# Performance work log

Hardware: AMD Instinct MI355X
Metric: run time of the kernel (lower is better)

## Reference

```python
import jax, jax.numpy as jnp
import numpy as np

B, H, S, D = 2, 16, 2048, 64  # depth = dmodel / num_heads
DMODEL = H * D


def setup_inputs() -> dict:
    key = jax.random.key(0)
    kq, kk, kv, kw = jax.random.split(key, 4)
    Q = jax.random.normal(kq, (B, H, S, D), dtype=jnp.float32)
    K = jax.random.normal(kk, (B, H, S, D), dtype=jnp.float32)
    V = jax.random.normal(kv, (B, H, S, D), dtype=jnp.float32)
    W = jax.random.normal(kw, (DMODEL, DMODEL), dtype=jnp.float32) * (1.0 / np.sqrt(DMODEL))
    b = jnp.zeros((DMODEL,), dtype=jnp.float32)
    return {"Q": Q, "K": K, "V": V, "W": W, "b": b}


def reference(Q, K, V, W, b):
    depth = Q.shape[-1]
    # scores: (B, H, S, S) -- full score matrix, matching the original math
    scores = jnp.einsum('bhqd,bhkd->bhqk', Q, K) / jnp.sqrt(jnp.float32(depth))
    attn = jax.nn.softmax(scores, axis=-1)
    vals = jnp.einsum('bhqk,bhkd->bhqd', attn, V)          # (B, H, S, D)
    vals = jnp.transpose(vals, (0, 2, 1, 3))               # (B, S, H, D)
    concat = vals.reshape(vals.shape[0], vals.shape[1], -1)  # (B, S, dmodel)
    return concat @ W + b
```

## Files before the change

### kernel.cpp

```cpp
#include <hip/hip_runtime.h>
#include <hip/hip_bf16.h>


typedef float  f32x16 __attribute__((ext_vector_type(16)));
typedef float  f32x4v __attribute__((ext_vector_type(4)));
typedef float  f32x2v __attribute__((ext_vector_type(2)));
typedef __bf16 bf16x8 __attribute__((ext_vector_type(8)));
typedef __bf16 bf16x4 __attribute__((ext_vector_type(4)));
typedef __bf16 bf16x2 __attribute__((ext_vector_type(2)));

static constexpr int Bn = 2, Hn = 16, Sn = 2048, Dn = 64, DM = 1024;
static constexpr size_t QKV_ELEMS = (size_t)Bn * Hn * Sn * Dn;

#define QSCALE 0.18033688011112042f

#if __has_builtin(__builtin_amdgcn_cvt_pk_bf16_f32)
static __device__ __forceinline__ unsigned pack2(float a, float b) {
  bf16x2 t = __builtin_amdgcn_cvt_pk_bf16_f32(a, b);
  union { bf16x2 v; unsigned u; } c; c.v = t; return c.u;
}
#else
static __device__ __forceinline__ unsigned pack2(float a, float b) {
  union { __bf16 h; unsigned short s; } ua, ub;
  ua.h = (__bf16)a; ub.h = (__bf16)b;
  return (unsigned)ua.s | ((unsigned)ub.s << 16);
}
#endif

static __device__ __forceinline__ void unzip8(const unsigned* wds, bf16x8* r0, bf16x8* r1) {
  union { unsigned u[4]; bf16x8 v; } a, b;
#pragma unroll
  for (int i = 0; i < 4; ++i) {
    unsigned lo = wds[2 * i], hi = wds[2 * i + 1];
    a.u[i] = (lo & 0xffffu) | (hi << 16);
    b.u[i] = (lo >> 16) | (hi & 0xffff0000u);
  }
  *r0 = a.v; *r1 = b.v;
}

__global__ __launch_bounds__(256) void convert_qk(
    const float* __restrict__ q, const float* __restrict__ k,
    __bf16* __restrict__ qo, __bf16* __restrict__ ko) {
  const int z = blockIdx.y;
  const float* src = z ? k : q;
  __bf16* dst      = z ? ko : qo;
  const float scale = z ? 1.0f : QSCALE;
  size_t i = ((size_t)blockIdx.x * 256 + threadIdx.x) * 8;
  f32x4v a = *(const f32x4v*)(src + i);
  f32x4v b = *(const f32x4v*)(src + i + 4);
  bf16x8 o;
#pragma unroll
  for (int j = 0; j < 4; ++j) { o[j] = (__bf16)(a[j] * scale); o[4 + j] = (__bf16)(b[j] * scale); }
  *(bf16x8*)(dst + i) = o;
}

__global__ __launch_bounds__(256) void convert_vt(const float* __restrict__ v,
                                                  __bf16* __restrict__ vt) {
  __shared__ __bf16 T[64][74];
  const int t = threadIdx.x, r = t >> 2, c0 = (t & 3) * 16;
  const int kv0 = blockIdx.x * 64, bh = blockIdx.y;
  const float* src = v + ((size_t)bh * Sn + kv0 + r) * Dn + c0;
  union { bf16x8 v8; unsigned u[4]; } o0, o1;
#pragma unroll
  for (int i = 0; i < 2; ++i) {
    f32x4v f = *(const f32x4v*)(src + i * 4);
#pragma unroll
    for (int j = 0; j < 4; ++j) o0.v8[i * 4 + j] = (__bf16)f[j];
  }
#pragma unroll
  for (int i = 0; i < 2; ++i) {
    f32x4v f = *(const f32x4v*)(src + 8 + i * 4);
#pragma unroll
    for (int j = 0; j < 4; ++j) o1.v8[i * 4 + j] = (__bf16)f[j];
  }
#pragma unroll
  for (int j = 0; j < 4; ++j) {
    *(unsigned*)&T[r][c0 + 2 * j]     = o0.u[j];
    *(unsigned*)&T[r][c0 + 8 + 2 * j] = o1.u[j];
  }
  __syncthreads();
  const int rp = t >> 3, k0 = (t & 7) * 8;
  unsigned wds[8];
#pragma unroll
  for (int i = 0; i < 8; ++i) wds[i] = *(const unsigned*)&T[k0 + i][2 * rp];
  bf16x8 r0, r1; unzip8(wds, &r0, &r1);
  __bf16* dst = vt + ((size_t)bh * Dn + 2 * rp) * Sn + kv0 + k0;
  *(bf16x8*)dst = r0;
  *(bf16x8*)(dst + Sn) = r1;
}

__global__ __launch_bounds__(256) void convert_w(const float* __restrict__ w,
                                                 __bf16* __restrict__ wt) {
  __shared__ __bf16 T[64][74];
  const int t = threadIdx.x, r = t >> 2, c0 = (t & 3) * 16;
  const int nt = blockIdx.x * 64, kt = blockIdx.y * 64;
  const float* src = w + (size_t)(kt + r) * DM + nt + c0;
  union { bf16x8 v8; unsigned u[4]; } o0, o1;
#pragma unroll
  for (int i = 0; i < 2; ++i) {
    f32x4v f = *(const f32x4v*)(src + i * 4);
#pragma unroll
    for (int j = 0; j < 4; ++j) o0.v8[i * 4 + j] = (__bf16)f[j];
  }
#pragma unroll
  for (int i = 0; i < 2; ++i) {
    f32x4v f = *(const f32x4v*)(src + 8 + i * 4);
#pragma unroll
    for (int j = 0; j < 4; ++j) o1.v8[i * 4 + j] = (__bf16)f[j];
  }
#pragma unroll
  for (int j = 0; j < 4; ++j) {
    *(unsigned*)&T[r][c0 + 2 * j]     = o0.u[j];
    *(unsigned*)&T[r][c0 + 8 + 2 * j] = o1.u[j];
  }
  __syncthreads();
  const int rp = t >> 3, k0 = (t & 7) * 8;
  unsigned wds[8];
#pragma unroll
  for (int i = 0; i < 8; ++i) wds[i] = *(const unsigned*)&T[k0 + i][2 * rp];
  bf16x8 r0, r1; unzip8(wds, &r0, &r1);
  __bf16* dst = wt + (size_t)(nt + 2 * rp) * DM + kt + k0;
  *(bf16x8*)dst = r0;
  *(bf16x8*)(dst + DM) = r1;
}

__global__ __launch_bounds__(256, 4) void attn(
    const __bf16* __restrict__ Qb, const __bf16* __restrict__ Kb,
    const __bf16* __restrict__ Vtg, __bf16* __restrict__ Cc) {
  const int tid = threadIdx.x;
  const int wave = tid >> 6, lane = tid & 63;
  const int ln = lane & 31, g = lane >> 5;
  const int qb = blockIdx.x, h = blockIdx.y, bz = blockIdx.z;

  __shared__ __bf16 Ks[2][64][72];
  __shared__ __bf16 Vs[2][64][72];

  const size_t hoff = (size_t)(bz * Hn + h) * Sn * Dn;
  const __bf16* Qp = Qb + hoff + (size_t)(qb * 128 + wave * 32) * Dn;
  const __bf16* Kp = Kb + hoff;
  const __bf16* Vp = Vtg + hoff;

  bf16x8 qf[4];
#pragma unroll
  for (int ks = 0; ks < 4; ++ks)
    qf[ks] = *(const bf16x8*)(Qp + (size_t)ln * Dn + ks * 16 + g * 8);

  const int sr = tid >> 2, sc = (tid & 3) * 16;
  const __bf16* kbase = Kp + (size_t)sr * Dn + sc;
  const __bf16* vbase = Vp + (size_t)sr * Sn + sc;

  bf16x8 k0r = *(const bf16x8*)kbase, k1r = *(const bf16x8*)(kbase + 8);
  bf16x8 v0r = *(const bf16x8*)vbase, v1r = *(const bf16x8*)(vbase + 8);
  *(bf16x8*)&Ks[0][sr][sc]     = k0r;
  *(bf16x8*)&Ks[0][sr][sc + 8] = k1r;
  *(bf16x8*)&Vs[0][sr][sc]     = v0r;
  *(bf16x8*)&Vs[0][sr][sc + 8] = v1r;
  k0r = *(const bf16x8*)(kbase + (size_t)64 * Dn);
  k1r = *(const bf16x8*)(kbase + (size_t)64 * Dn + 8);
  v0r = *(const bf16x8*)(vbase + 64);
  v1r = *(const bf16x8*)(vbase + 64 + 8);
  __syncthreads();

  f32x16 O0 = {}, O1 = {};
  float Lown = 0.0f;
  constexpr int NT = Sn / 64;

  for (int kt = 0; kt < NT; ++kt) {
    const int buf = kt & 1;

    float p[32];
#pragma unroll
    for (int mt = 0; mt < 2; ++mt) {
      f32x16 s = {};
#pragma unroll
      for (int ks = 0; ks < 4; ++ks) {
        bf16x8 kf = *(const bf16x8*)&Ks[buf][mt * 32 + ln][ks * 16 + g * 8];
        s = __builtin_amdgcn_mfma_f32_32x32x16_bf16(kf, qf[ks], s, 0, 0, 0);
      }
#pragma unroll
      for (int r = 0; r < 16; ++r) p[mt * 16 + r] = __builtin_amdgcn_exp2f(s[r]);
    }
    f32x2v s2 = {0.0f, 0.0f};
#pragma unroll
    for (int tt = 0; tt < 16; ++tt) {
      f32x2v t2 = {p[2 * tt], p[2 * tt + 1]};
      s2 += t2;
    }
    Lown += s2[0] + s2[1];

    unsigned w[16];
#pragma unroll
    for (int tt = 0; tt < 8; ++tt) {
      w[tt]     = pack2(p[2 * tt], p[2 * tt + 1]);
      w[8 + tt] = pack2(p[16 + 2 * tt], p[16 + 2 * tt + 1]);
    }

    if (kt + 1 < NT) {
      const int nb = buf ^ 1;
      *(bf16x8*)&Ks[nb][sr][sc]     = k0r;
      *(bf16x8*)&Ks[nb][sr][sc + 8] = k1r;
      *(bf16x8*)&Vs[nb][sr][sc]     = v0r;
      *(bf16x8*)&Vs[nb][sr][sc + 8] = v1r;
      if (kt + 2 < NT) {
        const __bf16* kp = kbase + (size_t)(kt + 2) * 64 * Dn;
        k0r = *(const bf16x8*)kp; k1r = *(const bf16x8*)(kp + 8);
        const __bf16* vp = vbase + (kt + 2) * 64;
        v0r = *(const bf16x8*)vp; v1r = *(const bf16x8*)(vp + 8);
      }
    }

#pragma unroll
    for (int s4 = 0; s4 < 4; ++s4) {
      const int wb = (s4 >> 1) * 8 + (s4 & 1) * 4;
      unsigned xs0 = g ? w[wb + 0] : w[wb + 2];
      unsigned xs1 = g ? w[wb + 1] : w[wb + 3];
      unsigned x0 = (unsigned)__shfl_xor((int)xs0, 32);
      unsigned x1 = (unsigned)__shfl_xor((int)xs1, 32);
      union { unsigned u[4]; bf16x8 v; } pu;
      pu.u[0] = g ? x0 : w[wb + 0];
      pu.u[1] = g ? x1 : w[wb + 1];
      pu.u[2] = g ? w[wb + 2] : x0;
      pu.u[3] = g ? w[wb + 3] : x1;
      bf16x8 vf0 = *(const bf16x8*)&Vs[buf][ln][s4 * 16 + g * 8];
      bf16x8 vf1 = *(const bf16x8*)&Vs[buf][32 + ln][s4 * 16 + g * 8];
      O0 = __builtin_amdgcn_mfma_f32_32x32x16_bf16(vf0, pu.v, O0, 0, 0, 0);
      O1 = __builtin_amdgcn_mfma_f32_32x32x16_bf16(vf1, pu.v, O1, 0, 0, 0);
    }
    __syncthreads();
  }

  const float Lfull = Lown + __shfl_xor(Lown, 32);
  const float inv = 1.0f / Lfull;
  __bf16* Osb = ((__bf16*)Ks) + wave * 32 * 72;
#pragma unroll
  for (int mtD = 0; mtD < 2; ++mtD) {
#pragma unroll
    for (int a = 0; a < 4; ++a) {
      const f32x16 O = mtD ? O1 : O0;
      bf16x4 t4;
#pragma unroll
      for (int c = 0; c < 4; ++c) t4[c] = (__bf16)(O[4 * a + c] * inv);
      *(bf16x4*)(Osb + ln * 72 + mtD * 32 + 8 * a + 4 * g) = t4;
    }
  }
  const int q0w = qb * 128 + wave * 32;
#pragma unroll
  for (int i = 0; i < 4; ++i) {
    const int rq = i * 8 + (lane >> 3);
    const int c8 = (lane & 7) * 8;
    bf16x8 o = *(const bf16x8*)(Osb + rq * 72 + c8);
    size_t base = (((size_t)bz * Sn + q0w + rq) * Hn + h) * Dn + c8;
    *(bf16x8*)&Cc[base] = o;
  }
}

__global__ __launch_bounds__(256, 2) void proj(
    const __bf16* __restrict__ A, const __bf16* __restrict__ Wt,
    const float* __restrict__ bias, float* __restrict__ out) {
  const int tid = threadIdx.x, wave = tid >> 6, lane = tid & 63;
  const int ln = lane & 31, g = lane >> 5;
  const int bm = blockIdx.x, bn = blockIdx.y;
  __shared__ __bf16 As[2][128][72];
  __shared__ __bf16 Bs[2][64][72];
  const int ar = tid >> 1, ac = (tid & 1) * 32;
  const int br = tid >> 2, bc = (tid & 3) * 16;
  f32x16 acc0 = {}, acc1 = {};
  const __bf16* Ap = A + (size_t)(bm * 128) * DM;
  const __bf16* Wp = Wt + (size_t)(bn * 64) * DM;

  bf16x8 a0, a1, a2, a3, b0, b1;
  {
    const __bf16* ap = Ap + (size_t)ar * DM + ac;
    a0 = *(const bf16x8*)ap;        a1 = *(const bf16x8*)(ap + 8);
    a2 = *(const bf16x8*)(ap + 16); a3 = *(const bf16x8*)(ap + 24);
    const __bf16* wp = Wp + (size_t)br * DM + bc;
    b0 = *(const bf16x8*)wp; b1 = *(const bf16x8*)(wp + 8);
  }
  *(bf16x8*)&As[0][ar][ac]      = a0;
  *(bf16x8*)&As[0][ar][ac + 8]  = a1;
  *(bf16x8*)&As[0][ar][ac + 16] = a2;
  *(bf16x8*)&As[0][ar][ac + 24] = a3;
  *(bf16x8*)&Bs[0][br][bc]      = b0;
  *(bf16x8*)&Bs[0][br][bc + 8]  = b1;
  {
    const __bf16* ap = Ap + (size_t)ar * DM + 64 + ac;
    a0 = *(const bf16x8*)ap;        a1 = *(const bf16x8*)(ap + 8);
    a2 = *(const bf16x8*)(ap + 16); a3 = *(const bf16x8*)(ap + 24);
    const __bf16* wp = Wp + (size_t)br * DM + 64 + bc;
    b0 = *(const bf16x8*)wp; b1 = *(const bf16x8*)(wp + 8);
  }
  __syncthreads();

  constexpr int KT = DM / 64;
  for (int kt = 0; kt < KT; ++kt) {
    const int buf = kt & 1;
#pragma unroll
    for (int ks = 0; ks < 4; ++ks) {
      bf16x8 af  = *(const bf16x8*)&As[buf][wave * 32 + ln][ks * 16 + g * 8];
      bf16x8 wf0 = *(const bf16x8*)&Bs[buf][ln][ks * 16 + g * 8];
      bf16x8 wf1 = *(const bf16x8*)&Bs[buf][32 + ln][ks * 16 + g * 8];
      acc0 = __builtin_amdgcn_mfma_f32_32x32x16_bf16(af, wf0, acc0, 0, 0, 0);
      acc1 = __builtin_amdgcn_mfma_f32_32x32x16_bf16(af, wf1, acc1, 0, 0, 0);
    }
    if (kt + 1 < KT) {
      const int nb = buf ^ 1;
      *(bf16x8*)&As[nb][ar][ac]      = a0;
      *(bf16x8*)&As[nb][ar][ac + 8]  = a1;
      *(bf16x8*)&As[nb][ar][ac + 16] = a2;
      *(bf16x8*)&As[nb][ar][ac + 24] = a3;
      *(bf16x8*)&Bs[nb][br][bc]      = b0;
      *(bf16x8*)&Bs[nb][br][bc + 8]  = b1;
      if (kt + 2 < KT) {
        const __bf16* ap = Ap + (size_t)ar * DM + (kt + 2) * 64 + ac;
        a0 = *(const bf16x8*)ap;        a1 = *(const bf16x8*)(ap + 8);
        a2 = *(const bf16x8*)(ap + 16); a3 = *(const bf16x8*)(ap + 24);
        const __bf16* wp = Wp + (size_t)br * DM + (kt + 2) * 64 + bc;
        b0 = *(const bf16x8*)wp; b1 = *(const bf16x8*)(wp + 8);
      }
    }
    __syncthreads();
  }
  float bv0 = bias[bn * 64 + ln], bv1 = bias[bn * 64 + 32 + ln];
#pragma unroll
  for (int r = 0; r < 16; ++r) {
    int row = bm * 128 + wave * 32 + (r & 3) + ((r >> 2) << 3) + (g << 2);
    out[(size_t)row * DM + bn * 64 + ln]      = acc0[r] + bv0;
    out[(size_t)row * DM + bn * 64 + 32 + ln] = acc1[r] + bv1;
  }
}

extern "C" void kernel_launch(void* const* d_in, const int* in_sizes, int n_in,
                              void* d_out, int out_size, void* d_ws, size_t ws_size,
                              hipStream_t stream) {
  const float* Q = (const float*)d_in[0];
  const float* K = (const float*)d_in[1];
  const float* V = (const float*)d_in[2];
  const float* W = (const float*)d_in[3];
  const float* b = (const float*)d_in[4];
  float* out = (float*)d_out;

  __bf16* ws  = (__bf16*)d_ws;
  __bf16* Qb  = ws;
  __bf16* Kb  = Qb + QKV_ELEMS;
  __bf16* Vtg = Kb + QKV_ELEMS;
  __bf16* Cc  = Vtg + QKV_ELEMS;
  __bf16* Wt  = Cc + QKV_ELEMS;

  convert_qk<<<dim3((unsigned)(QKV_ELEMS / (256 * 8)), 2, 1), 256, 0, stream>>>(Q, K, Qb, Kb);
  convert_vt<<<dim3(Sn / 64, Bn * Hn, 1), 256, 0, stream>>>(V, Vtg);
  convert_w<<<dim3(DM / 64, DM / 64, 1), 256, 0, stream>>>(W, Wt);
  attn<<<dim3(Sn / 128, Hn, Bn), 256, 0, stream>>>(Qb, Kb, Vtg, Cc);
  proj<<<dim3(Bn * Sn / 128, DM / 64, 1), 256, 0, stream>>>(Cc, Wt, b, out);
}
```

Baseline: 163.6 us.

## Split attention KV tiles across wave pairs and shrink projection tiles

```diff
diff --git a/kernel.cpp b/kernel.cpp
--- a/kernel.cpp
+++ b/kernel.cpp
@@ -124,19 +124,21 @@
   *(bf16x8*)(dst + DM) = r1;
 }
 
-__global__ __launch_bounds__(256, 4) void attn(
+__global__ __launch_bounds__(512, 4) void attn(
     const __bf16* __restrict__ Qb, const __bf16* __restrict__ Kb,
     const __bf16* __restrict__ Vtg, __bf16* __restrict__ Cc) {
   const int tid = threadIdx.x;
   const int wave = tid >> 6, lane = tid & 63;
   const int ln = lane & 31, g = lane >> 5;
+  const int qg = wave >> 1, kh = wave & 1;
   const int qb = blockIdx.x, h = blockIdx.y, bz = blockIdx.z;
 
-  __shared__ __bf16 Ks[2][64][72];
-  __shared__ __bf16 Vs[2][64][72];
+  __shared__ __bf16 smem[2][2][64][72];
+  __bf16 (*Ks)[64][72] = smem[0];
+  __bf16 (*Vs)[64][72] = smem[1];
 
   const size_t hoff = (size_t)(bz * Hn + h) * Sn * Dn;
-  const __bf16* Qp = Qb + hoff + (size_t)(qb * 128 + wave * 32) * Dn;
+  const __bf16* Qp = Qb + hoff + (size_t)(qb * 128 + qg * 32) * Dn;
   const __bf16* Kp = Kb + hoff;
   const __bf16* Vp = Vtg + hoff;
 
@@ -145,20 +147,16 @@
   for (int ks = 0; ks < 4; ++ks)
     qf[ks] = *(const bf16x8*)(Qp + (size_t)ln * Dn + ks * 16 + g * 8);
 
-  const int sr = tid >> 2, sc = (tid & 3) * 16;
+  const int sr = tid >> 3, sc = (tid & 7) * 8;
   const __bf16* kbase = Kp + (size_t)sr * Dn + sc;
   const __bf16* vbase = Vp + (size_t)sr * Sn + sc;
 
-  bf16x8 k0r = *(const bf16x8*)kbase, k1r = *(const bf16x8*)(kbase + 8);
-  bf16x8 v0r = *(const bf16x8*)vbase, v1r = *(const bf16x8*)(vbase + 8);
-  *(bf16x8*)&Ks[0][sr][sc]     = k0r;
-  *(bf16x8*)&Ks[0][sr][sc + 8] = k1r;
-  *(bf16x8*)&Vs[0][sr][sc]     = v0r;
-  *(bf16x8*)&Vs[0][sr][sc + 8] = v1r;
+  bf16x8 k0r = *(const bf16x8*)kbase;
+  bf16x8 v0r = *(const bf16x8*)vbase;
+  *(bf16x8*)&Ks[0][sr][sc] = k0r;
+  *(bf16x8*)&Vs[0][sr][sc] = v0r;
   k0r = *(const bf16x8*)(kbase + (size_t)64 * Dn);
-  k1r = *(const bf16x8*)(kbase + (size_t)64 * Dn + 8);
   v0r = *(const bf16x8*)(vbase + 64);
-  v1r = *(const bf16x8*)(vbase + 64 + 8);
   __syncthreads();
 
   f32x16 O0 = {}, O1 = {};
@@ -168,50 +166,37 @@
   for (int kt = 0; kt < NT; ++kt) {
     const int buf = kt & 1;
 
-    float p[32];
-#pragma unroll
-    for (int mt = 0; mt < 2; ++mt) {
-      f32x16 s = {};
-#pragma unroll
-      for (int ks = 0; ks < 4; ++ks) {
-        bf16x8 kf = *(const bf16x8*)&Ks[buf][mt * 32 + ln][ks * 16 + g * 8];
-        s = __builtin_amdgcn_mfma_f32_32x32x16_bf16(kf, qf[ks], s, 0, 0, 0);
-      }
-#pragma unroll
-      for (int r = 0; r < 16; ++r) p[mt * 16 + r] = __builtin_amdgcn_exp2f(s[r]);
-    }
+    f32x16 s = {};
+#pragma unroll
+    for (int ks = 0; ks < 4; ++ks) {
+      bf16x8 kf = *(const bf16x8*)&Ks[buf][kh * 32 + ln][ks * 16 + g * 8];
+      s = __builtin_amdgcn_mfma_f32_32x32x16_bf16(kf, qf[ks], s, 0, 0, 0);
+    }
+    float p[16];
+#pragma unroll
+    for (int r = 0; r < 16; ++r) p[r] = __builtin_amdgcn_exp2f(s[r]);
     f32x2v s2 = {0.0f, 0.0f};
 #pragma unroll
-    for (int tt = 0; tt < 16; ++tt) {
-      f32x2v t2 = {p[2 * tt], p[2 * tt + 1]};
-      s2 += t2;
-    }
+    for (int tt = 0; tt < 8; ++tt) { f32x2v t2 = {p[2 * tt], p[2 * tt + 1]}; s2 += t2; }
     Lown += s2[0] + s2[1];
 
-    unsigned w[16];
-#pragma unroll
-    for (int tt = 0; tt < 8; ++tt) {
-      w[tt]     = pack2(p[2 * tt], p[2 * tt + 1]);
-      w[8 + tt] = pack2(p[16 + 2 * tt], p[16 + 2 * tt + 1]);
-    }
+    unsigned w[8];
+#pragma unroll
+    for (int tt = 0; tt < 8; ++tt) w[tt] = pack2(p[2 * tt], p[2 * tt + 1]);
 
     if (kt + 1 < NT) {
       const int nb = buf ^ 1;
-      *(bf16x8*)&Ks[nb][sr][sc]     = k0r;
-      *(bf16x8*)&Ks[nb][sr][sc + 8] = k1r;
-      *(bf16x8*)&Vs[nb][sr][sc]     = v0r;
-      *(bf16x8*)&Vs[nb][sr][sc + 8] = v1r;
+      *(bf16x8*)&Ks[nb][sr][sc] = k0r;
+      *(bf16x8*)&Vs[nb][sr][sc] = v0r;
       if (kt + 2 < NT) {
-        const __bf16* kp = kbase + (size_t)(kt + 2) * 64 * Dn;
-        k0r = *(const bf16x8*)kp; k1r = *(const bf16x8*)(kp + 8);
-        const __bf16* vp = vbase + (kt + 2) * 64;
-        v0r = *(const bf16x8*)vp; v1r = *(const bf16x8*)(vp + 8);
+        k0r = *(const bf16x8*)(kbase + (size_t)(kt + 2) * 64 * Dn);
+        v0r = *(const bf16x8*)(vbase + (kt + 2) * 64);
       }
     }
 
 #pragma unroll
-    for (int s4 = 0; s4 < 4; ++s4) {
-      const int wb = (s4 >> 1) * 8 + (s4 & 1) * 4;
+    for (int s4 = 0; s4 < 2; ++s4) {
+      const int wb = s4 * 4;
       unsigned xs0 = g ? w[wb + 0] : w[wb + 2];
       unsigned xs1 = g ? w[wb + 1] : w[wb + 3];
       unsigned x0 = (unsigned)__shfl_xor((int)xs0, 32);
@@ -221,72 +206,103 @@
       pu.u[1] = g ? x1 : w[wb + 1];
       pu.u[2] = g ? w[wb + 2] : x0;
       pu.u[3] = g ? w[wb + 3] : x1;
-      bf16x8 vf0 = *(const bf16x8*)&Vs[buf][ln][s4 * 16 + g * 8];
-      bf16x8 vf1 = *(const bf16x8*)&Vs[buf][32 + ln][s4 * 16 + g * 8];
+      bf16x8 vf0 = *(const bf16x8*)&Vs[buf][ln][kh * 32 + s4 * 16 + g * 8];
+      bf16x8 vf1 = *(const bf16x8*)&Vs[buf][32 + ln][kh * 32 + s4 * 16 + g * 8];
       O0 = __builtin_amdgcn_mfma_f32_32x32x16_bf16(vf0, pu.v, O0, 0, 0, 0);
       O1 = __builtin_amdgcn_mfma_f32_32x32x16_bf16(vf1, pu.v, O1, 0, 0, 0);
     }
     __syncthreads();
   }
 
-  const float Lfull = Lown + __shfl_xor(Lown, 32);
-  const float inv = 1.0f / Lfull;
-  __bf16* Osb = ((__bf16*)Ks) + wave * 32 * 72;
-#pragma unroll
-  for (int mtD = 0; mtD < 2; ++mtD) {
-#pragma unroll
-    for (int a = 0; a < 4; ++a) {
-      const f32x16 O = mtD ? O1 : O0;
-      bf16x4 t4;
-#pragma unroll
-      for (int c = 0; c < 4; ++c) t4[c] = (__bf16)(O[4 * a + c] * inv);
-      *(bf16x4*)(Osb + ln * 72 + mtD * 32 + 8 * a + 4 * g) = t4;
-    }
-  }
-  const int q0w = qb * 128 + wave * 32;
-#pragma unroll
-  for (int i = 0; i < 4; ++i) {
-    const int rq = i * 8 + (lane >> 3);
+  const float Lred = Lown + __shfl_xor(Lown, 32);
+  float* Ex = (float*)smem;
+  const int slot = (qg * 64 + lane) * 36;
+  if (kh == 1) {
+#pragma unroll
+    for (int i = 0; i < 4; ++i) {
+      f32x4v t = {O0[4 * i], O0[4 * i + 1], O0[4 * i + 2], O0[4 * i + 3]};
+      *(f32x4v*)&Ex[slot + 4 * i] = t;
+    }
+#pragma unroll
+    for (int i = 0; i < 4; ++i) {
+      f32x4v t = {O1[4 * i], O1[4 * i + 1], O1[4 * i + 2], O1[4 * i + 3]};
+      *(f32x4v*)&Ex[slot + 16 + 4 * i] = t;
+    }
+    Ex[slot + 32] = Lred;
+  }
+  __syncthreads();
+  float inv = 0.0f;
+  if (kh == 0) {
+#pragma unroll
+    for (int i = 0; i < 4; ++i) {
+      f32x4v t = *(const f32x4v*)&Ex[slot + 4 * i];
+#pragma unroll
+      for (int c = 0; c < 4; ++c) O0[4 * i + c] += t[c];
+    }
+#pragma unroll
+    for (int i = 0; i < 4; ++i) {
+      f32x4v t = *(const f32x4v*)&Ex[slot + 16 + 4 * i];
+#pragma unroll
+      for (int c = 0; c < 4; ++c) O1[4 * i + c] += t[c];
+    }
+    inv = 1.0f / (Lred + Ex[slot + 32]);
+  }
+  __syncthreads();
+  __bf16* T = (__bf16*)smem;
+  if (kh == 0) {
+#pragma unroll
+    for (int dh = 0; dh < 2; ++dh) {
+#pragma unroll
+      for (int a = 0; a < 4; ++a) {
+        const f32x16 O = dh ? O1 : O0;
+        bf16x4 t4;
+#pragma unroll
+        for (int c = 0; c < 4; ++c) t4[c] = (__bf16)(O[4 * a + c] * inv);
+        *(bf16x4*)&T[(qg * 32 + ln) * 72 + dh * 32 + 8 * a + 4 * g] = t4;
+      }
+    }
+  }
+  __syncthreads();
+  const int q0 = qb * 128;
+#pragma unroll
+  for (int i = 0; i < 2; ++i) {
+    const int rq = wave * 16 + i * 8 + (lane >> 3);
     const int c8 = (lane & 7) * 8;
-    bf16x8 o = *(const bf16x8*)(Osb + rq * 72 + c8);
-    size_t base = (((size_t)bz * Sn + q0w + rq) * Hn + h) * Dn + c8;
+    bf16x8 o = *(const bf16x8*)&T[rq * 72 + c8];
+    size_t base = (((size_t)bz * Sn + q0 + rq) * Hn + h) * Dn + c8;
     *(bf16x8*)&Cc[base] = o;
   }
 }
 
-__global__ __launch_bounds__(256, 2) void proj(
+__global__ __launch_bounds__(256, 4) void proj(
     const __bf16* __restrict__ A, const __bf16* __restrict__ Wt,
     const float* __restrict__ bias, float* __restrict__ out) {
   const int tid = threadIdx.x, wave = tid >> 6, lane = tid & 63;
   const int ln = lane & 31, g = lane >> 5;
+  const int mh = wave >> 1, nh = wave & 1;
   const int bm = blockIdx.x, bn = blockIdx.y;
-  __shared__ __bf16 As[2][128][72];
+  __shared__ __bf16 As[2][64][72];
   __shared__ __bf16 Bs[2][64][72];
-  const int ar = tid >> 1, ac = (tid & 1) * 32;
-  const int br = tid >> 2, bc = (tid & 3) * 16;
-  f32x16 acc0 = {}, acc1 = {};
-  const __bf16* Ap = A + (size_t)(bm * 128) * DM;
+  const int ar = tid >> 2, ac = (tid & 3) * 16;
+  f32x16 acc = {};
+  const __bf16* Ap = A + (size_t)(bm * 64) * DM;
   const __bf16* Wp = Wt + (size_t)(bn * 64) * DM;
 
-  bf16x8 a0, a1, a2, a3, b0, b1;
+  bf16x8 a0, a1, b0, b1;
   {
     const __bf16* ap = Ap + (size_t)ar * DM + ac;
-    a0 = *(const bf16x8*)ap;        a1 = *(const bf16x8*)(ap + 8);
-    a2 = *(const bf16x8*)(ap + 16); a3 = *(const bf16x8*)(ap + 24);
-    const __bf16* wp = Wp + (size_t)br * DM + bc;
+    a0 = *(const bf16x8*)ap; a1 = *(const bf16x8*)(ap + 8);
+    const __bf16* wp = Wp + (size_t)ar * DM + ac;
     b0 = *(const bf16x8*)wp; b1 = *(const bf16x8*)(wp + 8);
   }
-  *(bf16x8*)&As[0][ar][ac]      = a0;
-  *(bf16x8*)&As[0][ar][ac + 8]  = a1;
-  *(bf16x8*)&As[0][ar][ac + 16] = a2;
-  *(bf16x8*)&As[0][ar][ac + 24] = a3;
-  *(bf16x8*)&Bs[0][br][bc]      = b0;
-  *(bf16x8*)&Bs[0][br][bc + 8]  = b1;
+  *(bf16x8*)&As[0][ar][ac]     = a0;
+  *(bf16x8*)&As[0][ar][ac + 8] = a1;
+  *(bf16x8*)&Bs[0][ar][ac]     = b0;
+  *(bf16x8*)&Bs[0][ar][ac + 8] = b1;
   {
     const __bf16* ap = Ap + (size_t)ar * DM + 64 + ac;
-    a0 = *(const bf16x8*)ap;        a1 = *(const bf16x8*)(ap + 8);
-    a2 = *(const bf16x8*)(ap + 16); a3 = *(const bf16x8*)(ap + 24);
-    const __bf16* wp = Wp + (size_t)br * DM + 64 + bc;
+    a0 = *(const bf16x8*)ap; a1 = *(const bf16x8*)(ap + 8);
+    const __bf16* wp = Wp + (size_t)ar * DM + 64 + ac;
     b0 = *(const bf16x8*)wp; b1 = *(const bf16x8*)(wp + 8);
   }
   __syncthreads();
@@ -296,36 +312,30 @@
     const int buf = kt & 1;
 #pragma unroll
     for (int ks = 0; ks < 4; ++ks) {
-      bf16x8 af  = *(const bf16x8*)&As[buf][wave * 32 + ln][ks * 16 + g * 8];
-      bf16x8 wf0 = *(const bf16x8*)&Bs[buf][ln][ks * 16 + g * 8];
-      bf16x8 wf1 = *(const bf16x8*)&Bs[buf][32 + ln][ks * 16 + g * 8];
-      acc0 = __builtin_amdgcn_mfma_f32_32x32x16_bf16(af, wf0, acc0, 0, 0, 0);
-      acc1 = __builtin_amdgcn_mfma_f32_32x32x16_bf16(af, wf1, acc1, 0, 0, 0);
+      bf16x8 af = *(const bf16x8*)&As[buf][mh * 32 + ln][ks * 16 + g * 8];
+      bf16x8 wf = *(const bf16x8*)&Bs[buf][nh * 32 + ln][ks * 16 + g * 8];
+      acc = __builtin_amdgcn_mfma_f32_32x32x16_bf16(af, wf, acc, 0, 0, 0);
     }
     if (kt + 1 < KT) {
       const int nb = buf ^ 1;
-      *(bf16x8*)&As[nb][ar][ac]      = a0;
-      *(bf16x8*)&As[nb][ar][ac + 8]  = a1;
-      *(bf16x8*)&As[nb][ar][ac + 16] = a2;
-      *(bf16x8*)&As[nb][ar][ac + 24] = a3;
-      *(bf16x8*)&Bs[nb][br][bc]      = b0;
-      *(bf16x8*)&Bs[nb][br][bc + 8]  = b1;
+      *(bf16x8*)&As[nb][ar][ac]     = a0;
+      *(bf16x8*)&As[nb][ar][ac + 8] = a1;
+      *(bf16x8*)&Bs[nb][ar][ac]     = b0;
+      *(bf16x8*)&Bs[nb][ar][ac + 8] = b1;
       if (kt + 2 < KT) {
         const __bf16* ap = Ap + (size_t)ar * DM + (kt + 2) * 64 + ac;
-        a0 = *(const bf16x8*)ap;        a1 = *(const bf16x8*)(ap + 8);
-        a2 = *(const bf16x8*)(ap + 16); a3 = *(const bf16x8*)(ap + 24);
-        const __bf16* wp = Wp + (size_t)br * DM + (kt + 2) * 64 + bc;
+        a0 = *(const bf16x8*)ap; a1 = *(const bf16x8*)(ap + 8);
+        const __bf16* wp = Wp + (size_t)ar * DM + (kt + 2) * 64 + ac;
         b0 = *(const bf16x8*)wp; b1 = *(const bf16x8*)(wp + 8);
       }
     }
     __syncthreads();
   }
-  float bv0 = bias[bn * 64 + ln], bv1 = bias[bn * 64 + 32 + ln];
+  const float bv = bias[bn * 64 + nh * 32 + ln];
 #pragma unroll
   for (int r = 0; r < 16; ++r) {
-    int row = bm * 128 + wave * 32 + (r & 3) + ((r >> 2) << 3) + (g << 2);
-    out[(size_t)row * DM + bn * 64 + ln]      = acc0[r] + bv0;
-    out[(size_t)row * DM + bn * 64 + 32 + ln] = acc1[r] + bv1;
+    int row = bm * 64 + mh * 32 + (r & 3) + 8 * (r >> 2) + 4 * g;
+    out[(size_t)row * DM + bn * 64 + nh * 32 + ln] = acc[r] + bv;
   }
 }
 
@@ -349,6 +359,6 @@
   convert_qk<<<dim3((unsigned)(QKV_ELEMS / (256 * 8)), 2, 1), 256, 0, stream>>>(Q, K, Qb, Kb);
   convert_vt<<<dim3(Sn / 64, Bn * Hn, 1), 256, 0, stream>>>(V, Vtg);
   convert_w<<<dim3(DM / 64, DM / 64, 1), 256, 0, stream>>>(W, Wt);
-  attn<<<dim3(Sn / 128, Hn, Bn), 256, 0, stream>>>(Qb, Kb, Vtg, Cc);
-  proj<<<dim3(Bn * Sn / 128, DM / 64, 1), 256, 0, stream>>>(Cc, Wt, b, out);
-}
+  attn<<<dim3(Sn / 128, Hn, Bn), 512, 0, stream>>>(Qb, Kb, Vtg, Cc);
+  proj<<<dim3(Bn * Sn / 64, DM / 64, 1), 256, 0, stream>>>(Cc, Wt, b, out);
+}
```

Result: no change. 164.8 us (+0.8%).

## Split attention waves across query groups and key halves; fuse conversion kernels

Applied to the files above, without the earlier changes.

```diff
diff --git a/kernel.cpp b/kernel.cpp
--- a/kernel.cpp
+++ b/kernel.cpp
@@ -38,45 +38,66 @@
   *r0 = a.v; *r1 = b.v;
 }
 
-__global__ __launch_bounds__(256) void convert_qk(
+__global__ __launch_bounds__(256) void convert_all(
     const float* __restrict__ q, const float* __restrict__ k,
-    __bf16* __restrict__ qo, __bf16* __restrict__ ko) {
-  const int z = blockIdx.y;
-  const float* src = z ? k : q;
-  __bf16* dst      = z ? ko : qo;
-  const float scale = z ? 1.0f : QSCALE;
-  size_t i = ((size_t)blockIdx.x * 256 + threadIdx.x) * 8;
-  f32x4v a = *(const f32x4v*)(src + i);
-  f32x4v b = *(const f32x4v*)(src + i + 4);
-  bf16x8 o;
-#pragma unroll
-  for (int j = 0; j < 4; ++j) { o[j] = (__bf16)(a[j] * scale); o[4 + j] = (__bf16)(b[j] * scale); }
-  *(bf16x8*)(dst + i) = o;
-}
-
-__global__ __launch_bounds__(256) void convert_vt(const float* __restrict__ v,
-                                                  __bf16* __restrict__ vt) {
+    const float* __restrict__ v, const float* __restrict__ w,
+    __bf16* __restrict__ qo, __bf16* __restrict__ ko,
+    __bf16* __restrict__ vt, __bf16* __restrict__ wt) {
   __shared__ __bf16 T[64][74];
-  const int t = threadIdx.x, r = t >> 2, c0 = (t & 3) * 16;
-  const int kv0 = blockIdx.x * 64, bh = blockIdx.y;
-  const float* src = v + ((size_t)bh * Sn + kv0 + r) * Dn + c0;
-  union { bf16x8 v8; unsigned u[4]; } o0, o1;
-#pragma unroll
-  for (int i = 0; i < 2; ++i) {
-    f32x4v f = *(const f32x4v*)(src + i * 4);
-#pragma unroll
-    for (int j = 0; j < 4; ++j) o0.v8[i * 4 + j] = (__bf16)f[j];
-  }
-#pragma unroll
-  for (int i = 0; i < 2; ++i) {
-    f32x4v f = *(const f32x4v*)(src + 8 + i * 4);
-#pragma unroll
-    for (int j = 0; j < 4; ++j) o1.v8[i * 4 + j] = (__bf16)f[j];
-  }
-#pragma unroll
-  for (int j = 0; j < 4; ++j) {
-    *(unsigned*)&T[r][c0 + 2 * j]     = o0.u[j];
-    *(unsigned*)&T[r][c0 + 8 + 2 * j] = o1.u[j];
+  const int bid = blockIdx.x, t = threadIdx.x;
+
+  if (bid < 4096) {
+    const int z = bid >> 11;
+    const int bx = bid & 2047;
+    const float* src = z ? k : q;
+    __bf16* dst      = z ? ko : qo;
+    const float scale = z ? 1.0f : QSCALE;
+    size_t i = ((size_t)bx * 256 + t) * 8;
+    f32x4v a = *(const f32x4v*)(src + i);
+    f32x4v b = *(const f32x4v*)(src + i + 4);
+    bf16x8 o;
+#pragma unroll
+    for (int j = 0; j < 4; ++j) { o[j] = (__bf16)(a[j] * scale); o[4 + j] = (__bf16)(b[j] * scale); }
+    *(bf16x8*)(dst + i) = o;
+    return;
+  }
+
+  const float* s0;
+  __bf16* dst0;
+  size_t dst_stride;
+  {
+    const int r = t >> 2, c0 = (t & 3) * 16;
+    if (bid < 5120) {
+      const int idx = bid - 4096;
+      const int kv0 = (idx & 31) * 64, bh = idx >> 5;
+      s0 = v + ((size_t)bh * Sn + kv0 + r) * Dn + c0;
+      dst0 = vt + (size_t)bh * Dn * Sn + kv0;
+      dst_stride = Sn;
+    } else {
+      const int idx = bid - 5120;
+      const int nt = (idx & 15) * 64, kt = (idx >> 4) * 64;
+      s0 = w + (size_t)(kt + r) * DM + nt + c0;
+      dst0 = wt + (size_t)nt * DM + kt;
+      dst_stride = DM;
+    }
+    union { bf16x8 v8; unsigned u[4]; } o0, o1;
+#pragma unroll
+    for (int i = 0; i < 2; ++i) {
+      f32x4v f = *(const f32x4v*)(s0 + i * 4);
+#pragma unroll
+      for (int j = 0; j < 4; ++j) o0.v8[i * 4 + j] = (__bf16)f[j];
+    }
+#pragma unroll
+    for (int i = 0; i < 2; ++i) {
+      f32x4v f = *(const f32x4v*)(s0 + 8 + i * 4);
+#pragma unroll
+      for (int j = 0; j < 4; ++j) o1.v8[i * 4 + j] = (__bf16)f[j];
+    }
+#pragma unroll
+    for (int j = 0; j < 4; ++j) {
+      *(unsigned*)&T[r][c0 + 2 * j]     = o0.u[j];
+      *(unsigned*)&T[r][c0 + 8 + 2 * j] = o1.u[j];
+    }
   }
   __syncthreads();
   const int rp = t >> 3, k0 = (t & 7) * 8;
@@ -84,66 +105,35 @@
 #pragma unroll
   for (int i = 0; i < 8; ++i) wds[i] = *(const unsigned*)&T[k0 + i][2 * rp];
   bf16x8 r0, r1; unzip8(wds, &r0, &r1);
-  __bf16* dst = vt + ((size_t)bh * Dn + 2 * rp) * Sn + kv0 + k0;
-  *(bf16x8*)dst = r0;
-  *(bf16x8*)(dst + Sn) = r1;
-}
-
-__global__ __launch_bounds__(256) void convert_w(const float* __restrict__ w,
-                                                 __bf16* __restrict__ wt) {
-  __shared__ __bf16 T[64][74];
-  const int t = threadIdx.x, r = t >> 2, c0 = (t & 3) * 16;
-  const int nt = blockIdx.x * 64, kt = blockIdx.y * 64;
-  const float* src = w + (size_t)(kt + r) * DM + nt + c0;
-  union { bf16x8 v8; unsigned u[4]; } o0, o1;
-#pragma unroll
-  for (int i = 0; i < 2; ++i) {
-    f32x4v f = *(const f32x4v*)(src + i * 4);
-#pragma unroll
-    for (int j = 0; j < 4; ++j) o0.v8[i * 4 + j] = (__bf16)f[j];
-  }
-#pragma unroll
-  for (int i = 0; i < 2; ++i) {
-    f32x4v f = *(const f32x4v*)(src + 8 + i * 4);
-#pragma unroll
-    for (int j = 0; j < 4; ++j) o1.v8[i * 4 + j] = (__bf16)f[j];
-  }
-#pragma unroll
-  for (int j = 0; j < 4; ++j) {
-    *(unsigned*)&T[r][c0 + 2 * j]     = o0.u[j];
-    *(unsigned*)&T[r][c0 + 8 + 2 * j] = o1.u[j];
-  }
-  __syncthreads();
-  const int rp = t >> 3, k0 = (t & 7) * 8;
-  unsigned wds[8];
-#pragma unroll
-  for (int i = 0; i < 8; ++i) wds[i] = *(const unsigned*)&T[k0 + i][2 * rp];
-  bf16x8 r0, r1; unzip8(wds, &r0, &r1);
-  __bf16* dst = wt + (size_t)(nt + 2 * rp) * DM + kt + k0;
-  *(bf16x8*)dst = r0;
-  *(bf16x8*)(dst + DM) = r1;
-}
-
-__global__ __launch_bounds__(256, 4) void attn(
+  __bf16* d0 = dst0 + (size_t)(2 * rp) * dst_stride + k0;
+  *(bf16x8*)d0 = r0;
+  *(bf16x8*)(d0 + dst_stride) = r1;
+}
+
+__global__ __launch_bounds__(256, 3) void attn(
     const __bf16* __restrict__ Qb, const __bf16* __restrict__ Kb,
     const __bf16* __restrict__ Vtg, __bf16* __restrict__ Cc) {
   const int tid = threadIdx.x;
   const int wave = tid >> 6, lane = tid & 63;
   const int ln = lane & 31, g = lane >> 5;
+  const int qg = wave >> 1, kh = wave & 1;
   const int qb = blockIdx.x, h = blockIdx.y, bz = blockIdx.z;
 
-  __shared__ __bf16 Ks[2][64][72];
-  __shared__ __bf16 Vs[2][64][72];
+  __shared__ __bf16 smem[2][2][64][72];
+  __bf16 (*Ks)[64][72] = smem[0];
+  __bf16 (*Vs)[64][72] = smem[1];
 
   const size_t hoff = (size_t)(bz * Hn + h) * Sn * Dn;
-  const __bf16* Qp = Qb + hoff + (size_t)(qb * 128 + wave * 32) * Dn;
+  const __bf16* Qp = Qb + hoff + (size_t)(qb * 128 + qg * 64) * Dn;
   const __bf16* Kp = Kb + hoff;
   const __bf16* Vp = Vtg + hoff;
 
-  bf16x8 qf[4];
-#pragma unroll
-  for (int ks = 0; ks < 4; ++ks)
-    qf[ks] = *(const bf16x8*)(Qp + (size_t)ln * Dn + ks * 16 + g * 8);
+  bf16x8 qf[2][4];
+#pragma unroll
+  for (int qt = 0; qt < 2; ++qt)
+#pragma unroll
+    for (int ks = 0; ks < 4; ++ks)
+      qf[qt][ks] = *(const bf16x8*)(Qp + (size_t)(qt * 32 + ln) * Dn + ks * 16 + g * 8);
 
   const int sr = tid >> 2, sc = (tid & 3) * 16;
   const __bf16* kbase = Kp + (size_t)sr * Dn + sc;
@@ -161,38 +151,34 @@
   v1r = *(const bf16x8*)(vbase + 64 + 8);
   __syncthreads();
 
-  f32x16 O0 = {}, O1 = {};
-  float Lown = 0.0f;
+  f32x16 O[2][2] = {{{}, {}}, {{}, {}}};
+  float Lown[2] = {0.0f, 0.0f};
   constexpr int NT = Sn / 64;
 
   for (int kt = 0; kt < NT; ++kt) {
     const int buf = kt & 1;
 
-    float p[32];
-#pragma unroll
-    for (int mt = 0; mt < 2; ++mt) {
+    bf16x8 kf[4];
+#pragma unroll
+    for (int ks = 0; ks < 4; ++ks)
+      kf[ks] = *(const bf16x8*)&Ks[buf][kh * 32 + ln][ks * 16 + g * 8];
+
+    unsigned w[2][8];
+#pragma unroll
+    for (int qt = 0; qt < 2; ++qt) {
       f32x16 s = {};
 #pragma unroll
-      for (int ks = 0; ks < 4; ++ks) {
-        bf16x8 kf = *(const bf16x8*)&Ks[buf][mt * 32 + ln][ks * 16 + g * 8];
-        s = __builtin_amdgcn_mfma_f32_32x32x16_bf16(kf, qf[ks], s, 0, 0, 0);
-      }
-#pragma unroll
-      for (int r = 0; r < 16; ++r) p[mt * 16 + r] = __builtin_amdgcn_exp2f(s[r]);
-    }
-    f32x2v s2 = {0.0f, 0.0f};
-#pragma unroll
-    for (int tt = 0; tt < 16; ++tt) {
-      f32x2v t2 = {p[2 * tt], p[2 * tt + 1]};
-      s2 += t2;
-    }
-    Lown += s2[0] + s2[1];
-
-    unsigned w[16];
-#pragma unroll
-    for (int tt = 0; tt < 8; ++tt) {
-      w[tt]     = pack2(p[2 * tt], p[2 * tt + 1]);
-      w[8 + tt] = pack2(p[16 + 2 * tt], p[16 + 2 * tt + 1]);
+      for (int ks = 0; ks < 4; ++ks)
+        s = __builtin_amdgcn_mfma_f32_32x32x16_bf16(kf[ks], qf[qt][ks], s, 0, 0, 0);
+      float p[16];
+#pragma unroll
+      for (int r = 0; r < 16; ++r) p[r] = __builtin_amdgcn_exp2f(s[r]);
+      f32x2v s2 = {0.0f, 0.0f};
+#pragma unroll
+      for (int tt = 0; tt < 8; ++tt) { f32x2v t2 = {p[2 * tt], p[2 * tt + 1]}; s2 += t2; }
+      Lown[qt] += s2[0] + s2[1];
+#pragma unroll
+      for (int tt = 0; tt < 8; ++tt) w[qt][tt] = pack2(p[2 * tt], p[2 * tt + 1]);
     }
 
     if (kt + 1 < NT) {
@@ -210,46 +196,86 @@
     }
 
 #pragma unroll
-    for (int s4 = 0; s4 < 4; ++s4) {
-      const int wb = (s4 >> 1) * 8 + (s4 & 1) * 4;
-      unsigned xs0 = g ? w[wb + 0] : w[wb + 2];
-      unsigned xs1 = g ? w[wb + 1] : w[wb + 3];
-      unsigned x0 = (unsigned)__shfl_xor((int)xs0, 32);
-      unsigned x1 = (unsigned)__shfl_xor((int)xs1, 32);
-      union { unsigned u[4]; bf16x8 v; } pu;
-      pu.u[0] = g ? x0 : w[wb + 0];
-      pu.u[1] = g ? x1 : w[wb + 1];
-      pu.u[2] = g ? w[wb + 2] : x0;
-      pu.u[3] = g ? w[wb + 3] : x1;
-      bf16x8 vf0 = *(const bf16x8*)&Vs[buf][ln][s4 * 16 + g * 8];
-      bf16x8 vf1 = *(const bf16x8*)&Vs[buf][32 + ln][s4 * 16 + g * 8];
-      O0 = __builtin_amdgcn_mfma_f32_32x32x16_bf16(vf0, pu.v, O0, 0, 0, 0);
-      O1 = __builtin_amdgcn_mfma_f32_32x32x16_bf16(vf1, pu.v, O1, 0, 0, 0);
+    for (int s4 = 0; s4 < 2; ++s4) {
+      const int cb = kh * 32 + s4 * 16 + g * 4;
+      union { bf16x4 h[2]; bf16x8 v; } vf0, vf1;
+      vf0.h[0] = *(const bf16x4*)&Vs[buf][ln][cb];
+      vf0.h[1] = *(const bf16x4*)&Vs[buf][ln][cb + 8];
+      vf1.h[0] = *(const bf16x4*)&Vs[buf][32 + ln][cb];
+      vf1.h[1] = *(const bf16x4*)&Vs[buf][32 + ln][cb + 8];
+#pragma unroll
+      for (int qt = 0; qt < 2; ++qt) {
+        union { unsigned u[4]; bf16x8 v; } pu;
+        pu.u[0] = w[qt][s4 * 4 + 0];
+        pu.u[1] = w[qt][s4 * 4 + 1];
+        pu.u[2] = w[qt][s4 * 4 + 2];
+        pu.u[3] = w[qt][s4 * 4 + 3];
+        O[qt][0] = __builtin_amdgcn_mfma_f32_32x32x16_bf16(vf0.v, pu.v, O[qt][0], 0, 0, 0);
+        O[qt][1] = __builtin_amdgcn_mfma_f32_32x32x16_bf16(vf1.v, pu.v, O[qt][1], 0, 0, 0);
+      }
     }
     __syncthreads();
   }
 
-  const float Lfull = Lown + __shfl_xor(Lown, 32);
-  const float inv = 1.0f / Lfull;
-  __bf16* Osb = ((__bf16*)Ks) + wave * 32 * 72;
-#pragma unroll
-  for (int mtD = 0; mtD < 2; ++mtD) {
-#pragma unroll
-    for (int a = 0; a < 4; ++a) {
-      const f32x16 O = mtD ? O1 : O0;
-      bf16x4 t4;
-#pragma unroll
-      for (int c = 0; c < 4; ++c) t4[c] = (__bf16)(O[4 * a + c] * inv);
-      *(bf16x4*)(Osb + ln * 72 + mtD * 32 + 8 * a + 4 * g) = t4;
-    }
-  }
-  const int q0w = qb * 128 + wave * 32;
+  float Lred[2];
+#pragma unroll
+  for (int qt = 0; qt < 2; ++qt) Lred[qt] = Lown[qt] + __shfl_xor(Lown[qt], 32);
+
+  float* Ex = (float*)smem;
+  const int slot = (qg * 64 + lane) * 68;
+  if (kh == 1) {
+#pragma unroll
+    for (int qt = 0; qt < 2; ++qt)
+#pragma unroll
+      for (int dh = 0; dh < 2; ++dh)
+#pragma unroll
+        for (int i = 0; i < 4; ++i) {
+          f32x4v t = {O[qt][dh][4 * i], O[qt][dh][4 * i + 1],
+                      O[qt][dh][4 * i + 2], O[qt][dh][4 * i + 3]};
+          *(f32x4v*)&Ex[slot + qt * 32 + dh * 16 + 4 * i] = t;
+        }
+    Ex[slot + 64] = Lred[0];
+    Ex[slot + 65] = Lred[1];
+  }
+  __syncthreads();
+  float inv[2] = {0.0f, 0.0f};
+  if (kh == 0) {
+#pragma unroll
+    for (int qt = 0; qt < 2; ++qt)
+#pragma unroll
+      for (int dh = 0; dh < 2; ++dh)
+#pragma unroll
+        for (int i = 0; i < 4; ++i) {
+          f32x4v t = *(const f32x4v*)&Ex[slot + qt * 32 + dh * 16 + 4 * i];
+#pragma unroll
+          for (int c = 0; c < 4; ++c) O[qt][dh][4 * i + c] += t[c];
+        }
+    inv[0] = 1.0f / (Lred[0] + Ex[slot + 64]);
+    inv[1] = 1.0f / (Lred[1] + Ex[slot + 65]);
+  }
+  __syncthreads();
+  __bf16* T = (__bf16*)smem;
+  if (kh == 0) {
+#pragma unroll
+    for (int qt = 0; qt < 2; ++qt)
+#pragma unroll
+      for (int dh = 0; dh < 2; ++dh)
+#pragma unroll
+        for (int a = 0; a < 4; ++a) {
+          bf16x4 t4;
+#pragma unroll
+          for (int c = 0; c < 4; ++c) t4[c] = (__bf16)(O[qt][dh][4 * a + c] * inv[qt]);
+          *(bf16x4*)&T[(qg * 64 + qt * 32 + ln) * 72 + dh * 32 + 8 * a + 4 * g] = t4;
+        }
+  }
+  __syncthreads();
+  const int q0 = qb * 128;
 #pragma unroll
   for (int i = 0; i < 4; ++i) {
-    const int rq = i * 8 + (lane >> 3);
-    const int c8 = (lane & 7) * 8;
-    bf16x8 o = *(const bf16x8*)(Osb + rq * 72 + c8);
-    size_t base = (((size_t)bz * Sn + q0w + rq) * Hn + h) * Dn + c8;
+    const int rq = i * 32 + (tid >> 3);
+    const int c8 = (tid & 7) * 8;
+    bf16x8 o = *(const bf16x8*)&T[rq * 72 + c8];
+    size_t base = (((size_t)bz * Sn + q0 + rq) * Hn + h) * Dn + c8;
     *(bf16x8*)&Cc[base] = o;
   }
 }
@@ -346,9 +372,7 @@
   __bf16* Cc  = Vtg + QKV_ELEMS;
   __bf16* Wt  = Cc + QKV_ELEMS;
 
-  convert_qk<<<dim3((unsigned)(QKV_ELEMS / (256 * 8)), 2, 1), 256, 0, stream>>>(Q, K, Qb, Kb);
-  convert_vt<<<dim3(Sn / 64, Bn * Hn, 1), 256, 0, stream>>>(V, Vtg);
-  convert_w<<<dim3(DM / 64, DM / 64, 1), 256, 0, stream>>>(W, Wt);
+  convert_all<<<dim3(5376, 1, 1), 256, 0, stream>>>(Q, K, V, W, Qb, Kb, Vtg, Wt);
   attn<<<dim3(Sn / 128, Hn, Bn), 256, 0, stream>>>(Qb, Kb, Vtg, Cc);
   proj<<<dim3(Bn * Sn / 128, DM / 64, 1), 256, 0, stream>>>(Cc, Wt, b, out);
 }
```

Result: faster. 159.2 us (-2.6%).
